# Optimization experiments

Measured on AMD Instinct MI355X. Metric: run time of the kernel, lower is better.

## Reference

```python
import jax, jax.numpy as jnp
import numpy as np

NQ = 20  # qubits per block
C64 = jnp.complex64
E0 = jnp.array([1.0 + 0.0j, 0.0 + 0.0j], dtype=C64)
PAULI_Z = jnp.array([[1.0, 0.0], [0.0, -1.0]], dtype=C64)


def rx(t):
    c = jnp.cos(t / 2).astype(C64)
    s = jnp.sin(t / 2).astype(C64)
    return jnp.stack([jnp.stack([c, -1j * s]), jnp.stack([-1j * s, c])])


def ry(t):
    c = jnp.cos(t / 2).astype(C64)
    s = jnp.sin(t / 2).astype(C64)
    return jnp.stack([jnp.stack([c, -s]), jnp.stack([s, c])])


def rz(t):
    e = jnp.exp((-0.5j) * t.astype(C64))  # exp(-i t/2)
    z = 0.0 * e
    return jnp.stack([jnp.stack([e, z]), jnp.stack([z, jnp.conj(e)])])


def apply_1q(psi, op, wire):
    # psi: flat 2**NQ statevector; op: 2x2 on `wire` (axis `wire` of (2,)*NQ view)
    psi = psi.reshape((2,) * NQ)
    psi = jnp.tensordot(op, psi, axes=[[1], [wire]])
    psi = jnp.moveaxis(psi, 0, wire)
    return psi.reshape(-1)


def apply_cnot(psi, c, t):
    psi = psi.reshape((2,) * NQ)
    idx0 = (slice(None),) * c + (slice(0, 1),)
    idx1 = (slice(None),) * c + (slice(1, 2),)
    a0 = psi[idx0]
    a1 = jnp.flip(psi[idx1], axis=t)
    return jnp.concatenate([a0, a1], axis=c).reshape(-1)


def _expect(psi, wire_ops):
    phi = psi
    for w, op in wire_ops:
        phi = apply_1q(phi, op, w)
    return jnp.real(jnp.vdot(psi, phi))


def _circuit(xs, pos_w, l1w, l2w):
    # xs: [16,4,3] angles for one image.
    # Heisenberg-pulled-back layer-2 observables: O_q = U_q^dag Z U_q,
    # U_q = RZ RY RX with layer_2_weights[q].
    Os = []
    for q in range(16):
        U = rz(l2w[q, 2]) @ (ry(l2w[q, 1]) @ rx(l2w[q, 0]))
        Os.append(U.conj().T @ PAULI_Z @ U)
    # Four independent 20-qubit block states after layer 1.
    psis = []
    for b in range(4):
        vecs = []
        for i in range(NQ):
            p = 4 * b + i // 5
            j = i % 5
            if j < 4:  # color qubit: RX,RY,RZ data encoding
                v = rz(xs[p, j, 2]) @ (ry(xs[p, j, 1]) @ (rx(xs[p, j, 0]) @ E0))
            else:  # spatial ancilla: RX,RY
                v = ry(pos_w[p, 1]) @ (rx(pos_w[p, 0]) @ E0)
            # layer-1 local rotations folded into the product state
            v = rz(l1w[i, 2]) @ (ry(l1w[i, 1]) @ (rx(l1w[i, 0]) @ v))
            vecs.append(v)
        psi = vecs[0]
        for v in vecs[1:]:
            psi = (psi[:, None] * v[None, :]).reshape(-1)
        for i in range(NQ):  # layer-1 CNOT ring within the block
            psi = apply_cnot(psi, i, (i + 1) % NQ)
        psis.append(psi)
    # Layer-2 CNOT-ring pullback: Z_{s0} -> Z_{s1..s15}; Z_{sk} -> Z_{s0..sk} (k=1..3).
    Efull = [_expect(psis[b], [(j, Os[4 * b + j]) for j in range(4)]) for b in range(4)]
    e0 = _expect(psis[0], [(j, Os[j]) for j in (1, 2, 3)]) * Efull[1] * Efull[2] * Efull[3]
    e1 = _expect(psis[0], [(0, Os[0]), (1, Os[1])])
    e2 = _expect(psis[0], [(0, Os[0]), (1, Os[1]), (2, Os[2])])
    e3 = Efull[0]
    return jnp.stack([e0, e1, e2, e3])


def setup_inputs() -> dict:
    key = jax.random.key(0)
    k1, k2, k3, k4, k5, k6 = jax.random.split(key, 6)
    B = 8
    return {
        "x": jax.random.normal(k1, (B, 16, 4, 3), dtype=jnp.float32),
        "pos_weights": jax.random.normal(k2, (16, 2), dtype=jnp.float32) * 0.01,
        "layer_1_weights": jax.random.normal(k3, (20, 3), dtype=jnp.float32) * 0.1,
        "layer_2_weights": jax.random.normal(k4, (16, 3), dtype=jnp.float32) * 0.1,
        "head_w": jax.random.normal(k5, (512, 4), dtype=jnp.float32) * 0.5,
        "head_b": jax.random.normal(k6, (512,), dtype=jnp.float32) * 0.1,
    }


def reference(x, pos_weights, layer_1_weights, layer_2_weights, head_w, head_b):
    q = jax.vmap(lambda xs: _circuit(xs, pos_weights, layer_1_weights, layer_2_weights))(x)  # [B,4]
    y = q @ head_w.T + head_b  # [B,512]
    n = jnp.linalg.norm(y, axis=-1, keepdims=True)
    return y / jnp.maximum(n, 1e-12)
```

## Files before the change

kernel.cpp:

```cpp
#include <hip/hip_runtime.h>
#include <math.h>


__device__ __forceinline__ void brx(float t, float& x, float& y, float& z) {
  float s, c; sincosf(t, &s, &c);
  float y2 = c * y - s * z;
  z = s * y + c * z;
  y = y2;
  (void)x;
}
__device__ __forceinline__ void bry(float t, float& x, float& y, float& z) {
  float s, c; sincosf(t, &s, &c);
  float z2 = c * z - s * x;
  x = s * z + c * x;
  z = z2;
  (void)y;
}
__device__ __forceinline__ void brz(float t, float& x, float& y, float& z) {
  float s, c; sincosf(t, &s, &c);
  float x2 = c * x - s * y;
  y = s * x + c * y;
  x = x2;
  (void)z;
}

__global__ __launch_bounds__(512) void qie_kernel(
    const float* __restrict__ x,
    const float* __restrict__ posw,
    const float* __restrict__ l1w,
    const float* __restrict__ l2w,
    const float* __restrict__ hw,
    const float* __restrict__ hb,
    float* __restrict__ out)
{
  const int img = blockIdx.x;
  const int tid = threadIdx.x;
  const int wid = tid >> 6, lane = tid & 63;

  __shared__ float bl[4][20][3];
  __shared__ float nv[16][3];
  __shared__ float eg[7];
  __shared__ float red[8];

  if (tid < 80) {
    const int b = tid / 20, i = tid % 20;
    const int p = 4 * b + i / 5, j = i % 5;
    float nx = 0.f, ny = 0.f, nz = 1.f;
    if (j < 4) {
      const float* a = x + ((img * 16 + p) * 4 + j) * 3;
      brx(a[0], nx, ny, nz);
      bry(a[1], nx, ny, nz);
      brz(a[2], nx, ny, nz);
    } else {
      brx(posw[p * 2 + 0], nx, ny, nz);
      bry(posw[p * 2 + 1], nx, ny, nz);
    }
    brx(l1w[i * 3 + 0], nx, ny, nz);
    bry(l1w[i * 3 + 1], nx, ny, nz);
    brz(l1w[i * 3 + 2], nx, ny, nz);
    bl[b][i][0] = nx; bl[b][i][1] = ny; bl[b][i][2] = nz;
  } else if (tid < 96) {
    const int q = tid - 80;
    float sa, ca, sb, cb;
    sincosf(l2w[q * 3 + 0], &sa, &ca);
    sincosf(l2w[q * 3 + 1], &sb, &cb);
    nv[q][0] = -sb;
    nv[q][1] = sa * cb;
    nv[q][2] = ca * cb;
  }
  __syncthreads();

  float acc = 0.0f;
  if (wid < 7) {
    const int g_nw[7] = {4, 4, 4, 4, 3, 2, 3};
    const int g_qb[7] = {0, 1, 2, 3, 0, 0, 0};
    const int g_w0[7] = {0, 0, 0, 0, 1, 0, 0};
    const int nw = g_nw[wid], qb = g_qb[wid], w0 = g_w0[wid];
    int nstr = 1;
    for (int k = 0; k < nw; ++k) nstr *= 3;
    for (int t = lane; t < nstr; t += 64) {
      unsigned xm = 0, zm = 0;
      float coeff = 1.0f;
      int tt = t;
      for (int k = 0; k < nw; ++k) {
        const int w = w0 + k;
        const int d = tt % 3;
        tt /= 3;
        coeff *= nv[4 * qb + w][d];
        if (d != 2) xm |= 1u << w;
        if (d != 0) zm |= 1u << w;
      }
      unsigned sgn = 0;
      for (int c = 19; c >= 0; --c) {
        const int tq = (c + 1) % 20;
        const unsigned xc = (xm >> c) & 1u, zc = (zm >> c) & 1u;
        const unsigned xt = (xm >> tq) & 1u, zt = (zm >> tq) & 1u;
        sgn ^= xc & zt & (xt ^ zc ^ 1u);
        xm ^= xc << tq;
        zm ^= zt << c;
      }
      float val = sgn ? -coeff : coeff;
      for (int i = 0; i < 20; ++i) {
        const unsigned xi = (xm >> i) & 1u, zi = (zm >> i) & 1u;
        if (xi | zi) val *= bl[qb][i][xi ? (zi ? 1 : 0) : 2];
      }
      acc += val;
    }
  }
  for (int off = 32; off; off >>= 1) acc += __shfl_xor(acc, off, 64);
  if (wid < 7 && lane == 0) eg[wid] = acc;
  __syncthreads();

  const float q0 = eg[4] * eg[1] * eg[2] * eg[3];
  const float q1 = eg[5];
  const float q2 = eg[6];
  const float q3 = eg[0];

  float y = q0 * hw[tid * 4 + 0] + q1 * hw[tid * 4 + 1] +
            q2 * hw[tid * 4 + 2] + q3 * hw[tid * 4 + 3] + hb[tid];
  float ss = y * y;
  for (int off = 32; off; off >>= 1) ss += __shfl_xor(ss, off, 64);
  if (lane == 0) red[wid] = ss;
  __syncthreads();
  float s = red[0] + red[1] + red[2] + red[3] + red[4] + red[5] + red[6] + red[7];
  const float rn = 1.0f / fmaxf(sqrtf(s), 1e-12f);
  out[img * 512 + tid] = y * rn;
}

extern "C" void kernel_launch(void* const* d_in, const int* in_sizes, int n_in,
                              void* d_out, int out_size, void* d_ws, size_t ws_size,
                              hipStream_t stream) {
  const float* x    = (const float*)d_in[0];
  const float* posw = (const float*)d_in[1];
  const float* l1w  = (const float*)d_in[2];
  const float* l2w  = (const float*)d_in[3];
  const float* hw   = (const float*)d_in[4];
  const float* hb   = (const float*)d_in[5];
  float* out = (float*)d_out;
  qie_kernel<<<8, 512, 0, stream>>>(x, posw, l1w, l2w, hw, hb, out);
}
```

Measured before the change: 12.76 us.

## Compute per-wave Bloch vectors locally to drop block barrier, prefetch head weights

Each of the seven working waves now computes its own block's Bloch vectors and observable vectors into wave-private shared memory and synchronises with a wave barrier instead of a block-wide __syncthreads. This removes one block-level barrier and lets the head weight and bias loads be issued at kernel start so their latency overlaps the Pauli-string work. The product loop over qubits now iterates only over set bits of the support mask. The cost is redundant trig work, since block 0's vectors are recomputed by four waves, plus more shared memory.

```diff
diff --git a/kernel.cpp b/kernel.cpp
--- a/kernel.cpp
+++ b/kernel.cpp
@@ -37,45 +37,58 @@
   const int tid = threadIdx.x;
   const int wid = tid >> 6, lane = tid & 63;
 
-  __shared__ float bl[4][20][3];
-  __shared__ float nv[16][3];
+  const float hw0 = hw[tid * 4 + 0];
+  const float hw1 = hw[tid * 4 + 1];
+  const float hw2 = hw[tid * 4 + 2];
+  const float hw3 = hw[tid * 4 + 3];
+  const float hbb = hb[tid];
+
+  __shared__ float wbl[7][20][3];
+  __shared__ float wnv[7][4][3];
   __shared__ float eg[7];
   __shared__ float red[8];
 
-  if (tid < 80) {
-    const int b = tid / 20, i = tid % 20;
-    const int p = 4 * b + i / 5, j = i % 5;
-    float nx = 0.f, ny = 0.f, nz = 1.f;
-    if (j < 4) {
-      const float* a = x + ((img * 16 + p) * 4 + j) * 3;
-      brx(a[0], nx, ny, nz);
-      bry(a[1], nx, ny, nz);
-      brz(a[2], nx, ny, nz);
-    } else {
-      brx(posw[p * 2 + 0], nx, ny, nz);
-      bry(posw[p * 2 + 1], nx, ny, nz);
-    }
-    brx(l1w[i * 3 + 0], nx, ny, nz);
-    bry(l1w[i * 3 + 1], nx, ny, nz);
-    brz(l1w[i * 3 + 2], nx, ny, nz);
-    bl[b][i][0] = nx; bl[b][i][1] = ny; bl[b][i][2] = nz;
-  } else if (tid < 96) {
-    const int q = tid - 80;
-    float sa, ca, sb, cb;
-    sincosf(l2w[q * 3 + 0], &sa, &ca);
-    sincosf(l2w[q * 3 + 1], &sb, &cb);
-    nv[q][0] = -sb;
-    nv[q][1] = sa * cb;
-    nv[q][2] = ca * cb;
-  }
-  __syncthreads();
+  const int g_nw[7] = {4, 4, 4, 4, 3, 2, 3};
+  const int g_qb[7] = {0, 1, 2, 3, 0, 0, 0};
+  const int g_w0[7] = {0, 0, 0, 0, 1, 0, 0};
 
   float acc = 0.0f;
   if (wid < 7) {
-    const int g_nw[7] = {4, 4, 4, 4, 3, 2, 3};
-    const int g_qb[7] = {0, 1, 2, 3, 0, 0, 0};
-    const int g_w0[7] = {0, 0, 0, 0, 1, 0, 0};
     const int nw = g_nw[wid], qb = g_qb[wid], w0 = g_w0[wid];
+
+    if (lane < 20) {
+      const int i = lane;
+      const int p = 4 * qb + i / 5, j = i % 5;
+      float nx = 0.f, ny = 0.f, nz = 1.f;
+      if (j < 4) {
+        const float* a = x + ((img * 16 + p) * 4 + j) * 3;
+        brx(a[0], nx, ny, nz);
+        bry(a[1], nx, ny, nz);
+        brz(a[2], nx, ny, nz);
+      } else {
+        brx(posw[p * 2 + 0], nx, ny, nz);
+        bry(posw[p * 2 + 1], nx, ny, nz);
+      }
+      brx(l1w[i * 3 + 0], nx, ny, nz);
+      bry(l1w[i * 3 + 1], nx, ny, nz);
+      brz(l1w[i * 3 + 2], nx, ny, nz);
+      wbl[wid][i][0] = nx; wbl[wid][i][1] = ny; wbl[wid][i][2] = nz;
+    } else if (lane < 24) {
+      const int k = lane - 20;
+      if (k < nw) {
+        const int q = 4 * qb + w0 + k;
+        float sa, ca, sb, cb;
+        sincosf(l2w[q * 3 + 0], &sa, &ca);
+        sincosf(l2w[q * 3 + 1], &sb, &cb);
+        wnv[wid][k][0] = -sb;
+        wnv[wid][k][1] = sa * cb;
+        wnv[wid][k][2] = ca * cb;
+      }
+    }
+    __builtin_amdgcn_wave_barrier();
+    asm volatile("s_waitcnt lgkmcnt(0)" ::: "memory");
+    __builtin_amdgcn_sched_barrier(0);
+
     int nstr = 1;
     for (int k = 0; k < nw; ++k) nstr *= 3;
     for (int t = lane; t < nstr; t += 64) {
@@ -86,7 +99,7 @@
         const int w = w0 + k;
         const int d = tt % 3;
         tt /= 3;
-        coeff *= nv[4 * qb + w][d];
+        coeff *= wnv[wid][k][d];
         if (d != 2) xm |= 1u << w;
         if (d != 0) zm |= 1u << w;
       }
@@ -100,9 +113,12 @@
         zm ^= zt << c;
       }
       float val = sgn ? -coeff : coeff;
-      for (int i = 0; i < 20; ++i) {
+      unsigned um = xm | zm;
+      while (um) {
+        const int i = __builtin_ctz(um);
+        um &= um - 1;
         const unsigned xi = (xm >> i) & 1u, zi = (zm >> i) & 1u;
-        if (xi | zi) val *= bl[qb][i][xi ? (zi ? 1 : 0) : 2];
+        val *= wbl[wid][i][xi ? (zi ? 1 : 0) : 2];
       }
       acc += val;
     }
@@ -116,13 +132,12 @@
   const float q2 = eg[6];
   const float q3 = eg[0];
 
-  float y = q0 * hw[tid * 4 + 0] + q1 * hw[tid * 4 + 1] +
-            q2 * hw[tid * 4 + 2] + q3 * hw[tid * 4 + 3] + hb[tid];
+  float y = q0 * hw0 + q1 * hw1 + q2 * hw2 + q3 * hw3 + hbb;
   float ss = y * y;
   for (int off = 32; off; off >>= 1) ss += __shfl_xor(ss, off, 64);
   if (lane == 0) red[wid] = ss;
   __syncthreads();
-  float s = red[0] + red[1] + red[2] + red[3] + red[4] + red[5] + red[6] + red[7];
+  const float s = red[0] + red[1] + red[2] + red[3] + red[4] + red[5] + red[6] + red[7];
   const float rn = 1.0f / fmaxf(sqrtf(s), 1e-12f);
   out[img * 512 + tid] = y * rn;
 }
```

Result: slower. 13.17 us (+3.2%).

## Precompute Pauli-string CNOT propagation table at compile time and prefetch head weights

Applied to the files above, without the earlier changes.

Moves the input-independent Pauli string enumeration and CNOT-ring sign/mask propagation into a constexpr device table, so each lane loads precomputed masks instead of running a 20-step loop. The product loop iterates only over set bits via ctz, and head weights and bias are loaded at kernel start to overlap with the earlier phases. This trades per-thread integer work for global constant loads and adds more register pressure.

```diff
diff --git a/kernel.cpp b/kernel.cpp
--- a/kernel.cpp
+++ b/kernel.cpp
@@ -1,6 +1,48 @@
 #include <hip/hip_runtime.h>
 #include <math.h>
 
+
+struct STab {
+  unsigned lo[7][128];
+  unsigned hi[7][128];
+};
+
+constexpr STab make_tab() {
+  STab T{};
+  const int g_nw[7] = {4, 4, 4, 4, 3, 2, 3};
+  const int g_w0[7] = {0, 0, 0, 0, 1, 0, 0};
+  for (int g = 0; g < 7; ++g) {
+    const int nw = g_nw[g], w0 = g_w0[g];
+    int nstr = 1;
+    for (int k = 0; k < nw; ++k) nstr *= 3;
+    for (int t = 0; t < nstr; ++t) {
+      unsigned xm = 0, zm = 0, dg = 0;
+      int tt = t;
+      for (int k = 0; k < nw; ++k) {
+        const int d = tt % 3;
+        tt /= 3;
+        dg |= (unsigned)d << (2 * k);
+        const int w = w0 + k;
+        if (d != 2) xm |= 1u << w;
+        if (d != 0) zm |= 1u << w;
+      }
+      unsigned sgn = 0;
+      for (int c = 19; c >= 0; --c) {
+        const int tq = (c + 1) % 20;
+        const unsigned xc = (xm >> c) & 1u, zc = (zm >> c) & 1u;
+        const unsigned xt = (xm >> tq) & 1u, zt = (zm >> tq) & 1u;
+        sgn ^= xc & zt & (xt ^ zc ^ 1u);
+        xm ^= xc << tq;
+        zm ^= zt << c;
+      }
+      T.lo[g][t] = xm | (sgn << 20) | (dg << 21);
+      T.hi[g][t] = zm;
+    }
+  }
+  return T;
+}
+
+__device__ constexpr STab TAB = make_tab();
 
 __device__ __forceinline__ void brx(float t, float& x, float& y, float& z) {
   float s, c; sincosf(t, &s, &c);
@@ -36,6 +78,19 @@
   const int img = blockIdx.x;
   const int tid = threadIdx.x;
   const int wid = tid >> 6, lane = tid & 63;
+
+  const float hw0 = hw[tid * 4 + 0];
+  const float hw1 = hw[tid * 4 + 1];
+  const float hw2 = hw[tid * 4 + 2];
+  const float hw3 = hw[tid * 4 + 3];
+  const float hbb = hb[tid];
+  unsigned lo1 = 0, hi1 = 0, lo2 = 0, hi2 = 0;
+  if (wid < 7) {
+    lo1 = TAB.lo[wid][lane];
+    hi1 = TAB.hi[wid][lane];
+    lo2 = TAB.lo[wid][lane + 64];
+    hi2 = TAB.hi[wid][lane + 64];
+  }
 
   __shared__ float bl[4][20][3];
   __shared__ float nv[16][3];
@@ -75,37 +130,28 @@
     const int g_nw[7] = {4, 4, 4, 4, 3, 2, 3};
     const int g_qb[7] = {0, 1, 2, 3, 0, 0, 0};
     const int g_w0[7] = {0, 0, 0, 0, 1, 0, 0};
-    const int nw = g_nw[wid], qb = g_qb[wid], w0 = g_w0[wid];
-    int nstr = 1;
-    for (int k = 0; k < nw; ++k) nstr *= 3;
-    for (int t = lane; t < nstr; t += 64) {
-      unsigned xm = 0, zm = 0;
+    const int g_ns[7] = {81, 81, 81, 81, 27, 9, 27};
+    const int nw = g_nw[wid], qb = g_qb[wid], w0 = g_w0[wid], nstr = g_ns[wid];
+
+    auto eval = [&](unsigned lo, unsigned hi) -> float {
       float coeff = 1.0f;
-      int tt = t;
-      for (int k = 0; k < nw; ++k) {
-        const int w = w0 + k;
-        const int d = tt % 3;
-        tt /= 3;
-        coeff *= nv[4 * qb + w][d];
-        if (d != 2) xm |= 1u << w;
-        if (d != 0) zm |= 1u << w;
+      const unsigned dg = lo >> 21;
+      for (int k = 0; k < nw; ++k)
+        coeff *= nv[4 * qb + w0 + k][(dg >> (2 * k)) & 3u];
+      float val = ((lo >> 20) & 1u) ? -coeff : coeff;
+      const unsigned xm = lo & 0xFFFFFu, zm = hi;
+      unsigned um = xm | zm;
+      while (um) {
+        const int i = __builtin_ctz(um);
+        um &= um - 1;
+        const unsigned xi = (xm >> i) & 1u, zi = (zm >> i) & 1u;
+        val *= bl[qb][i][xi ? (zi ? 1 : 0) : 2];
       }
-      unsigned sgn = 0;
-      for (int c = 19; c >= 0; --c) {
-        const int tq = (c + 1) % 20;
-        const unsigned xc = (xm >> c) & 1u, zc = (zm >> c) & 1u;
-        const unsigned xt = (xm >> tq) & 1u, zt = (zm >> tq) & 1u;
-        sgn ^= xc & zt & (xt ^ zc ^ 1u);
-        xm ^= xc << tq;
-        zm ^= zt << c;
-      }
-      float val = sgn ? -coeff : coeff;
-      for (int i = 0; i < 20; ++i) {
-        const unsigned xi = (xm >> i) & 1u, zi = (zm >> i) & 1u;
-        if (xi | zi) val *= bl[qb][i][xi ? (zi ? 1 : 0) : 2];
-      }
-      acc += val;
-    }
+      return val;
+    };
+
+    if (lane < nstr) acc = eval(lo1, hi1);
+    if (lane + 64 < nstr) acc += eval(lo2, hi2);
   }
   for (int off = 32; off; off >>= 1) acc += __shfl_xor(acc, off, 64);
   if (wid < 7 && lane == 0) eg[wid] = acc;
@@ -116,13 +162,12 @@
   const float q2 = eg[6];
   const float q3 = eg[0];
 
-  float y = q0 * hw[tid * 4 + 0] + q1 * hw[tid * 4 + 1] +
-            q2 * hw[tid * 4 + 2] + q3 * hw[tid * 4 + 3] + hb[tid];
+  float y = q0 * hw0 + q1 * hw1 + q2 * hw2 + q3 * hw3 + hbb;
   float ss = y * y;
   for (int off = 32; off; off >>= 1) ss += __shfl_xor(ss, off, 64);
   if (lane == 0) red[wid] = ss;
   __syncthreads();
-  float s = red[0] + red[1] + red[2] + red[3] + red[4] + red[5] + red[6] + red[7];
+  const float s = red[0] + red[1] + red[2] + red[3] + red[4] + red[5] + red[6] + red[7];
   const float rn = 1.0f / fmaxf(sqrtf(s), 1e-12f);
   out[img * 512 + tid] = y * rn;
 }
```

After: 11.92 us. 1.07x faster.
